# Kernel tuning notes

Measured on AMD Instinct MI355X. Metric: run time of the kernel, lower is better.

Reference implementation:

```python
import jax, jax.numpy as jnp
import numpy as np

D = 100          # graph size d
DIST = 10        # band distance
PI_ARG = 10.0    # args.pi
TOL = 1e-4       # args.tol
HID = 64         # hid_dim of each TApproximator
NP_ = int(HID * 0.2)   # 12 periodic units
NS_ = HID - NP_        # 52 sigmoid units

# banded off-diagonal positions in row-major order (matches reshape_B loop)
_pairs = [(r, c) for r in range(D) for c in range(D)
          if -DIST <= c - r <= DIST and r != c]
E = len(_pairs)  # = D*D - D - (D-DIST)*(D-DIST-1) = 1890
ROWS = jnp.array([p[0] for p in _pairs], dtype=jnp.int32)
COLS = jnp.array([p[1] for p in _pairs], dtype=jnp.int32)

N = 2048  # number of time points


def setup_inputs() -> dict:
    key = jax.random.key(0)
    ks = jax.random.split(key, 11)
    def lin(k, shape, fan_in):
        return jax.random.uniform(k, shape, jnp.float32, -1.0, 1.0) / np.sqrt(fan_in)
    return {
        "T":      jax.random.normal(ks[0], (N,), jnp.float32),
        "W1":     lin(ks[1], (E, NS_), 1),        # fc1 weight (input is scalar)
        "b1":     lin(ks[2], (E, NS_), 1),
        "W1p":    lin(ks[3], (E, NP_), 1),        # fc1_ weight
        "b1p":    lin(ks[4], (E, NP_), 1),
        "W2":     lin(ks[5], (E, HID, HID), HID), # fc2 weight [E, in, out]
        "b2":     lin(ks[6], (E, HID), HID),
        "W3":     lin(ks[7], (E, HID), HID),      # fc3 weight
        "b3":     lin(ks[8], (E,), HID),
        "beta":   jnp.ones((E,), jnp.float32),    # nn.Parameter([1.0]) per edge
        "bias_p": jnp.ones((E,), jnp.float32),    # nn.Parameter([1.0]) per edge
    }


def reference(T, W1, b1, W1p, b1p, W2, b2, W3, b3, beta, bias_p):
    # All E tiny MLPs evaluated as one batched pass. T: [N]
    t = T[:, None, None]                                   # [N,1,1]
    x1 = jax.nn.sigmoid(t * W1[None] + b1[None])           # [N,E,52]
    lin2 = t * W1p[None] + b1p[None]                       # [N,E,12]
    x2 = jnp.cos(beta[None, :, None] * jnp.pi * lin2 / PI_ARG
                 + bias_p[None, :, None])                  # [N,E,12]
    h = jax.nn.sigmoid(jnp.concatenate([x1, x2], axis=-1)) # [N,E,64] (double sigmoid on x1 path, as in source)
    h = jax.nn.sigmoid(jnp.einsum('neh,ehk->nek', h, W2) + b2[None])  # [N,E,64]
    out = jnp.einsum('neh,eh->ne', h, W3) + b3[None]       # [N,E]
    out = jnp.where(jnp.abs(out) < TOL, 0.0, out)          # masked_fill sparsify
    # reshape_B: scatter banded entries into [N, D, D]
    B = jnp.zeros((T.shape[0], D, D), dtype=out.dtype).at[:, ROWS, COLS].set(out)
    return B
```

## Files before the change

### kernel.cpp

```cpp
#include <hip/hip_runtime.h>
#include <hip/hip_bf16.h>
#include <stdint.h>

#define D_DIM  100
#define DISTW  10
#define E_NUM  1890
#define HID    64
#define NSIG   52
#define NPF    12
#define N_ROWS 2048
#define ITERS  (N_ROWS / 64)
#define TOLV   1e-4f
#define MAT    (D_DIM * D_DIM)
#define TOT_ELEMS (N_ROWS * MAT)
#define ZB     512
#define ZPER   (TOT_ELEMS / ZB)

#define TS        1024
#define F_SCALE   (TS / 13.0f)
#define F_OFF     (TS * 0.5f + 0.5f)
#define E_SCALE   (TS / 16.0f)
#define E_CONST   (TS * 0.5f + 0.5f + 2.0f * TS)

typedef __attribute__((ext_vector_type(8))) short bf16x8;
typedef __attribute__((ext_vector_type(4))) float f32x4;
typedef __attribute__((ext_vector_type(2))) float f32x2;

__device__ __forceinline__ float fast_exp2(float x) { return __builtin_amdgcn_exp2f(x); }
__device__ __forceinline__ float fast_rcp(float x)  { return __builtin_amdgcn_rcpf(x); }
__device__ __forceinline__ float fast_cosr(float x) { return __builtin_amdgcn_cosf(x); }

__device__ __forceinline__ float sigmoid_exact(float x) {
    return fast_rcp(1.0f + fast_exp2(x * -1.44269504f));
}

__device__ __forceinline__ short f2bf(float x) {
    __hip_bfloat16 h = __float2bfloat16(x);
    return __builtin_bit_cast(short, h);
}

__device__ __forceinline__ float dpp_sum16(float v) {
    int x;
    x = __builtin_amdgcn_update_dpp(0, __builtin_bit_cast(int, v), 0x118, 0xF, 0xF, true);
    v += __builtin_bit_cast(float, x);
    x = __builtin_amdgcn_update_dpp(0, __builtin_bit_cast(int, v), 0x114, 0xF, 0xF, true);
    v += __builtin_bit_cast(float, x);
    x = __builtin_amdgcn_update_dpp(0, __builtin_bit_cast(int, v), 0x112, 0xF, 0xF, true);
    v += __builtin_bit_cast(float, x);
    x = __builtin_amdgcn_update_dpp(0, __builtin_bit_cast(int, v), 0x111, 0xF, 0xF, true);
    v += __builtin_bit_cast(float, x);
    return v;
}

#define FEAT_PAIR(AF, K, TV) {                                              \
    f32x2 x2 = (f32x2){(TV), (TV)} * cw[K] + cb[K];                         \
    uint32_t b0 = ((uint32_t)x2.x) << 2;                                    \
    uint32_t b1 = ((uint32_t)x2.y) << 2;                                    \
    AF[(K) >> 2][2 * ((K) & 3)]     = f2bf(*(const float*)(lutB + b0));     \
    AF[(K) >> 2][2 * ((K) & 3) + 1] = f2bf(*(const float*)(lutB + b1)); }
#define FEAT16(AF, TV) { FEAT_PAIR(AF,0,TV) FEAT_PAIR(AF,1,TV)              \
    FEAT_PAIR(AF,2,TV) FEAT_PAIR(AF,3,TV) FEAT_PAIR(AF,4,TV)                \
    FEAT_PAIR(AF,5,TV) FEAT_PAIR(AF,6,TV) FEAT_PAIR(AF,7,TV) }

#define MM8(ACC, AF) {                                                      \
    _Pragma("unroll")                                                       \
    for (int ct = 0; ct < 4; ++ct)                                          \
        ACC[ct] = (f32x4){b2v[ct], b2v[ct], b2v[ct], b2v[ct]};              \
    _Pragma("unroll")                                                       \
    for (int ct = 0; ct < 4; ++ct) {                                        \
        ACC[ct] = __builtin_amdgcn_mfma_f32_16x16x32_bf16(AF[0], bfrag[0][ct], ACC[ct], 0, 0, 0); \
        ACC[ct] = __builtin_amdgcn_mfma_f32_16x16x32_bf16(AF[1], bfrag[1][ct], ACC[ct], 0, 0, 0); \
    } }

#define EPI(ACC, N0) {                                                      \
    f32x4 ix[4];                                                            \
    _Pragma("unroll")                                                       \
    for (int ct = 0; ct < 4; ++ct)                                          \
        ix[ct] = ACC[ct] * (f32x4){E_SCALE,E_SCALE,E_SCALE,E_SCALE}         \
               + (f32x4){E_CONST,E_CONST,E_CONST,E_CONST};                  \
    float p[4];                                                             \
    _Pragma("unroll")                                                       \
    for (int reg = 0; reg < 4; ++reg) {                                     \
        float s = 0.0f;                                                     \
        _Pragma("unroll")                                                   \
        for (int ct = 0; ct < 4; ++ct) {                                    \
            uint32_t bi = ((uint32_t)ix[ct][reg]) << 2;                     \
            s = fmaf(*(const float*)(lutB + bi), w3v[ct], s);               \
        }                                                                   \
        p[reg] = dpp_sum16(s);                                              \
    }                                                                       \
    if (lm == 15) {                                                         \
        _Pragma("unroll")                                                   \
        for (int r = 0; r < 4; ++r) {                                       \
            float out = p[r] + bias3;                                       \
            if (fabsf(out) < TOLV) out = 0.0f;                              \
            int row = (N0) + 4 * g + r;                                     \
            Bout[(size_t)row * MAT + rcoff] = out;                          \
        }                                                                   \
    } }

__global__ __launch_bounds__(256)
void golem_kernel(const float* __restrict__ T,   const float* __restrict__ W1,
                  const float* __restrict__ b1,  const float* __restrict__ W1p,
                  const float* __restrict__ b1p, const float* __restrict__ W2,
                  const float* __restrict__ b2,  const float* __restrict__ W3,
                  const float* __restrict__ b3,  const float* __restrict__ beta,
                  const float* __restrict__ bias_p, float* __restrict__ Bout)
{
    const int tid = threadIdx.x;

    if (blockIdx.x >= E_NUM) {
        const int zb = (int)blockIdx.x - E_NUM;
        const size_t base = (size_t)zb * ZPER;
        for (int off = tid * 4; off < ZPER; off += 256 * 4) {
            const size_t i = base + off;
            const int cell = (int)(i % MAT);
            const int r = cell / D_DIM;
            const int c = cell - r * D_DIM;
            const bool fast = (c <= D_DIM - 4) && ((c + 3 < r - DISTW) || (c > r + DISTW));
            if (fast) {
                *reinterpret_cast<f32x4*>(Bout + i) = (f32x4){0.0f, 0.0f, 0.0f, 0.0f};
            } else {
                #pragma unroll
                for (int k = 0; k < 4; ++k) {
                    const size_t j = i + k;
                    const int cell2 = (int)(j % MAT);
                    const int r2 = cell2 / D_DIM;
                    const int c2 = cell2 - r2 * D_DIM;
                    const int d = c2 - r2;
                    const bool band = (d >= -DISTW) && (d <= DISTW) && (d != 0);
                    if (!band) Bout[j] = 0.0f;
                }
            }
        }
        return;
    }

    const int e    = blockIdx.x;
    const int lane = tid & 63;
    const int wave = tid >> 6;
    const int g    = lane >> 4;
    const int lm   = lane & 15;

    __shared__ float sLut[3 * TS];
    __shared__ float sTT[N_ROWS];
    __shared__ float sWA[HID], sWB[HID], sW3[HID], sB2[HID];
    __shared__ float sScal[1];
    __shared__ int   sRC;

    for (int i = tid; i < N_ROWS; i += 256) sTT[i] = T[i];

    {
        const float cc1 = beta[e] * 0.05f;
        const float cc2 = bias_p[e] * 0.15915494309f;
        for (int i = tid; i < TS; i += 256) {
            float x  = (i - (TS / 2)) * (13.0f / TS);
            sLut[i]          = sigmoid_exact(sigmoid_exact(x));
            sLut[TS + i]     = sigmoid_exact(fast_cosr(fmaf(x, cc1, cc2)));
            float xe = (i - (TS / 2)) * (16.0f / TS);
            sLut[2 * TS + i] = sigmoid_exact(xe);
        }
    }

    if (tid < HID) {
        float wa, wb;
        if (tid < NSIG) { wa = W1 [e * NSIG + tid];         wb = b1 [e * NSIG + tid]; }
        else            { wa = W1p[e * NPF + (tid - NSIG)]; wb = b1p[e * NPF + (tid - NSIG)]; }
        sWA[tid] = wa; sWB[tid] = wb;
        sW3[tid] = W3[e * HID + tid];
        sB2[tid] = b2[e * HID + tid];
    }
    if (tid == 0) {
        sScal[0] = b3[e];
        int r = 0, off = 0;
        for (;;) {
            int lo = r - DISTW; if (lo < 0) lo = 0;
            int hi = r + DISTW; if (hi > D_DIM - 1) hi = D_DIM - 1;
            int cnt = hi - lo;
            if (e < off + cnt) {
                int idx = e - off;
                int c = lo + idx;
                if (c >= r) c += 1;
                sRC = r * D_DIM + c;
                break;
            }
            off += cnt; ++r;
        }
    }
    __syncthreads();

    const float* W2e = W2 + (size_t)e * (HID * HID);
    bf16x8 bfrag[2][4];
    #pragma unroll
    for (int kk = 0; kk < 2; ++kk)
        #pragma unroll
        for (int ct = 0; ct < 4; ++ct)
            #pragma unroll
            for (int j = 0; j < 8; ++j)
                bfrag[kk][ct][j] = f2bf(W2e[(8 * g + j + 32 * kk) * HID + 16 * ct + lm]);

    f32x2 cw[8], cb[8];
    #pragma unroll
    for (int k = 0; k < 8; ++k) {
        int q = k >> 2, j0 = 2 * (k & 3);
        int c0 = 8 * g + j0 + 32 * q;
        float base0 = F_OFF + ((c0     < NSIG) ? 0.0f : (float)TS);
        float base1 = F_OFF + ((c0 + 1 < NSIG) ? 0.0f : (float)TS);
        cw[k] = (f32x2){sWA[c0] * F_SCALE, sWA[c0 + 1] * F_SCALE};
        cb[k] = (f32x2){fmaf(sWB[c0], F_SCALE, base0), fmaf(sWB[c0 + 1], F_SCALE, base1)};
    }

    float b2v[4], w3v[4];
    #pragma unroll
    for (int ct = 0; ct < 4; ++ct) {
        b2v[ct] = sB2[16 * ct + lm];
        w3v[ct] = sW3[16 * ct + lm];
    }
    const float bias3 = sScal[0];
    const int   rcoff = sRC;
    const char* lutB  = (const char*)sLut;
    const int   rbase = wave * 16;

    bf16x8 afA[2], afB[2];
    {
        float t0 = sTT[rbase + lm];
        FEAT16(afA, t0);
    }
    for (int it = 0; it < ITERS; it += 2) {
        {
            f32x4 acc[4];
            MM8(acc, afA);
            float tB = sTT[(it + 1) * 64 + rbase + lm];
            FEAT16(afB, tB);
            EPI(acc, it * 64 + rbase);
        }
        {
            f32x4 acc[4];
            MM8(acc, afB);
            if (it < ITERS - 2) {
                float tA = sTT[(it + 2) * 64 + rbase + lm];
                FEAT16(afA, tA);
            }
            EPI(acc, (it + 1) * 64 + rbase);
        }
    }
}

extern "C" void kernel_launch(void* const* d_in, const int* in_sizes, int n_in,
                              void* d_out, int out_size, void* d_ws, size_t ws_size,
                              hipStream_t stream) {
    const float* T      = (const float*)d_in[0];
    const float* W1     = (const float*)d_in[1];
    const float* b1     = (const float*)d_in[2];
    const float* W1p    = (const float*)d_in[3];
    const float* b1p    = (const float*)d_in[4];
    const float* W2     = (const float*)d_in[5];
    const float* b2     = (const float*)d_in[6];
    const float* W3     = (const float*)d_in[7];
    const float* b3     = (const float*)d_in[8];
    const float* beta   = (const float*)d_in[9];
    const float* bias_p = (const float*)d_in[10];
    float* Bout = (float*)d_out;

    golem_kernel<<<dim3(E_NUM + ZB), dim3(256), 0, stream>>>(
        T, W1, b1, W1p, b1p, W2, b2, W3, b3, beta, bias_p, Bout);
}
```

Before: 134.4 us.

## Split time rows across two grid halves and compute epilogue sigmoid directly

Launches a 2D grid so that each edge block handles half of the time points. This doubles the block count and halves the per-block loop, with the zero-fill blocks split the same way. The epilogue sigmoid LUT lookup is replaced by a direct exp2/rcp sigmoid, and T is read straight from global memory instead of being staged in shared memory. The trade-off is that the per-edge LUT and weight setup is now repeated in twice as many blocks, and the epilogue does more transcendental work per element in exchange for less LDS traffic and occupancy.

```diff
diff --git a/kernel.cpp b/kernel.cpp
--- a/kernel.cpp
+++ b/kernel.cpp
@@ -9,18 +9,16 @@
 #define NSIG   52
 #define NPF    12
 #define N_ROWS 2048
-#define ITERS  (N_ROWS / 64)
+#define NHALF  1024
+#define ITERS  (NHALF / 64)
 #define TOLV   1e-4f
 #define MAT    (D_DIM * D_DIM)
-#define TOT_ELEMS (N_ROWS * MAT)
-#define ZB     512
-#define ZPER   (TOT_ELEMS / ZB)
+#define HALF_ELEMS (NHALF * MAT)
+#define ZB     256
 
 #define TS        1024
 #define F_SCALE   (TS / 13.0f)
 #define F_OFF     (TS * 0.5f + 0.5f)
-#define E_SCALE   (TS / 16.0f)
-#define E_CONST   (TS * 0.5f + 0.5f + 2.0f * TS)
 
 typedef __attribute__((ext_vector_type(8))) short bf16x8;
 typedef __attribute__((ext_vector_type(4))) float f32x4;
@@ -73,20 +71,13 @@
     } }
 
 #define EPI(ACC, N0) {                                                      \
-    f32x4 ix[4];                                                            \
-    _Pragma("unroll")                                                       \
-    for (int ct = 0; ct < 4; ++ct)                                          \
-        ix[ct] = ACC[ct] * (f32x4){E_SCALE,E_SCALE,E_SCALE,E_SCALE}         \
-               + (f32x4){E_CONST,E_CONST,E_CONST,E_CONST};                  \
     float p[4];                                                             \
     _Pragma("unroll")                                                       \
     for (int reg = 0; reg < 4; ++reg) {                                     \
         float s = 0.0f;                                                     \
         _Pragma("unroll")                                                   \
-        for (int ct = 0; ct < 4; ++ct) {                                    \
-            uint32_t bi = ((uint32_t)ix[ct][reg]) << 2;                     \
-            s = fmaf(*(const float*)(lutB + bi), w3v[ct], s);               \
-        }                                                                   \
+        for (int ct = 0; ct < 4; ++ct)                                      \
+            s = fmaf(sigmoid_exact(ACC[ct][reg]), w3v[ct], s);              \
         p[reg] = dpp_sum16(s);                                              \
     }                                                                       \
     if (lm == 15) {                                                         \
@@ -107,12 +98,14 @@
                   const float* __restrict__ b3,  const float* __restrict__ beta,
                   const float* __restrict__ bias_p, float* __restrict__ Bout)
 {
-    const int tid = threadIdx.x;
+    const int tid  = threadIdx.x;
+    const int half = blockIdx.y;
 
     if (blockIdx.x >= E_NUM) {
-        const int zb = (int)blockIdx.x - E_NUM;
-        const size_t base = (size_t)zb * ZPER;
-        for (int off = tid * 4; off < ZPER; off += 256 * 4) {
+        const int zb  = (int)blockIdx.x - E_NUM;
+        const int per = HALF_ELEMS / ZB;
+        const size_t base = (size_t)half * HALF_ELEMS + (size_t)zb * per;
+        for (int off = tid * 4; off < per; off += 256 * 4) {
             const size_t i = base + off;
             const int cell = (int)(i % MAT);
             const int r = cell / D_DIM;
@@ -142,23 +135,18 @@
     const int g    = lane >> 4;
     const int lm   = lane & 15;
 
-    __shared__ float sLut[3 * TS];
-    __shared__ float sTT[N_ROWS];
+    __shared__ float sLut[2 * TS];
     __shared__ float sWA[HID], sWB[HID], sW3[HID], sB2[HID];
     __shared__ float sScal[1];
     __shared__ int   sRC;
-
-    for (int i = tid; i < N_ROWS; i += 256) sTT[i] = T[i];
 
     {
         const float cc1 = beta[e] * 0.05f;
         const float cc2 = bias_p[e] * 0.15915494309f;
         for (int i = tid; i < TS; i += 256) {
             float x  = (i - (TS / 2)) * (13.0f / TS);
-            sLut[i]          = sigmoid_exact(sigmoid_exact(x));
-            sLut[TS + i]     = sigmoid_exact(fast_cosr(fmaf(x, cc1, cc2)));
-            float xe = (i - (TS / 2)) * (16.0f / TS);
-            sLut[2 * TS + i] = sigmoid_exact(xe);
+            sLut[i]      = sigmoid_exact(sigmoid_exact(x));
+            sLut[TS + i] = sigmoid_exact(fast_cosr(fmaf(x, cc1, cc2)));
         }
     }
 
@@ -219,29 +207,29 @@
     const float bias3 = sScal[0];
     const int   rcoff = sRC;
     const char* lutB  = (const char*)sLut;
-    const int   rbase = wave * 16;
+    const float* Tg = T + half * NHALF + wave * 16 + lm;
 
     bf16x8 afA[2], afB[2];
     {
-        float t0 = sTT[rbase + lm];
+        float t0 = Tg[0];
         FEAT16(afA, t0);
     }
     for (int it = 0; it < ITERS; it += 2) {
         {
             f32x4 acc[4];
             MM8(acc, afA);
-            float tB = sTT[(it + 1) * 64 + rbase + lm];
+            float tB = Tg[(it + 1) * 64];
             FEAT16(afB, tB);
-            EPI(acc, it * 64 + rbase);
+            EPI(acc, half * NHALF + it * 64 + wave * 16);
         }
         {
             f32x4 acc[4];
             MM8(acc, afB);
             if (it < ITERS - 2) {
-                float tA = sTT[(it + 2) * 64 + rbase + lm];
+                float tA = Tg[(it + 2) * 64];
                 FEAT16(afA, tA);
             }
-            EPI(acc, (it + 1) * 64 + rbase);
+            EPI(acc, half * NHALF + (it + 1) * 64 + wave * 16);
         }
     }
 }
@@ -262,6 +250,6 @@
     const float* bias_p = (const float*)d_in[10];
     float* Bout = (float*)d_out;
 
-    golem_kernel<<<dim3(E_NUM + ZB), dim3(256), 0, stream>>>(
+    golem_kernel<<<dim3(E_NUM + ZB, 2), dim3(256), 0, stream>>>(
         T, W1, b1, W1p, b1p, W2, b2, W3, b3, beta, bias_p, Bout);
 }
```

New measurement: 135.4 us. Within noise of the previous version (+0.7%).
